# Performance work log

Measured on AMD Instinct MI355X. Metric: run time of the kernel, lower is better.

## Reference

```python
import jax, jax.numpy as jnp
import numpy as np

NUM_HEADS = 16  # init kwarg num_attention_heads


def setup_inputs() -> dict:
    key = jax.random.key(0)
    k1, k2, k3, k4 = jax.random.split(key, 4)
    B, T, E = 2, 2048, 1024
    query = jax.random.normal(k1, (B, T, E), dtype=jnp.float32)
    key_t = jax.random.normal(k2, (B, T, E), dtype=jnp.float32)
    value = jax.random.normal(k3, (B, T, E), dtype=jnp.float32)
    # final output projection (nn.Linear(hidden, hidden, bias=False)); torch stores [out,in]
    W_out = jax.random.normal(k4, (E, E), dtype=jnp.float32) * 0.02
    return {"query": query, "key": key_t, "value": value, "W_out": W_out}


def reference(query, key, value, W_out):
    # NOTE: in the source, the per-head q_i/k_i/v_i linear projections are
    # overwritten by reshapes of the raw inputs, so the qs/ks/vs weights are
    # dead code. Every head computes identical output; mean over heads is a
    # no-op. We reproduce that exact math here.
    B, T, E = query.shape
    H = NUM_HEADS
    d = E // H  # head_dim; also d_k used in the 1/sqrt(d_k) scaling

    def split_heads(x):  # [B,T,E] -> [B,H,T,d]
        return x.reshape(B, T, H, d).transpose(0, 2, 1, 3)

    q = split_heads(query)
    k = split_heads(key)
    v = split_heads(value)

    scale = jnp.sqrt(jnp.asarray(d, dtype=jnp.float32))
    scores = jnp.einsum('bhtd,bhsd->bhts', q, k) / scale  # [B,H,T,T]
    attn = jax.nn.softmax(scores, axis=-1)
    head = jnp.einsum('bhts,bhsd->bhtd', attn, v)         # [B,H,T,d]
    head = head.transpose(0, 2, 1, 3).reshape(B, T, E)    # concat heads

    # mean over H identical head outputs == head; final linear (no bias)
    outputs = head @ W_out.T                              # [B,T,E]
    # mean over H identical attention maps == attn, returned as [B*H,T,T]
    attention = attn.reshape(B * H, T, T)
    return outputs, attention
```

## Files before the change

kernel.cpp:

```cpp
#include <hip/hip_runtime.h>
#include <hip/hip_fp16.h>

#define B_NUM  2
#define T_DIM  2048
#define E_DIM  1024
#define H_NUM  16
#define D_HEAD 64
#define BH_NUM (B_NUM * H_NUM)
#define NT     (T_DIM / 64)

using half8  = __attribute__((ext_vector_type(8))) _Float16;
using half4v = __attribute__((ext_vector_type(4))) _Float16;
using f32x4  = __attribute__((ext_vector_type(4))) float;

#define AS1 __attribute__((address_space(1)))
#define AS3 __attribute__((address_space(3)))

#define QSCALE 0.18033688011112042f

#define BAR_VM(N)                                                       \
    do {                                                                \
        asm volatile("s_waitcnt vmcnt(" #N ")" ::: "memory");           \
        __builtin_amdgcn_s_barrier();                                   \
        __builtin_amdgcn_sched_barrier(0);                              \
    } while (0)

__device__ __forceinline__ void bar_plain() {
    __builtin_amdgcn_s_barrier();
    __builtin_amdgcn_sched_barrier(0);
}

__global__ void cast_all_kernel(const float* __restrict__ kin,
                                const float* __restrict__ win,
                                _Float16* __restrict__ Kh,
                                _Float16* __restrict__ Wh,
                                int nk4, int ntot4) {
    int stride = gridDim.x * blockDim.x;
    for (int i = blockIdx.x * blockDim.x + threadIdx.x; i < ntot4; i += stride) {
        const float* src = (i < nk4) ? kin : win;
        _Float16* dst    = (i < nk4) ? Kh  : Wh;
        int j            = (i < nk4) ? i   : i - nk4;
        float4 v = reinterpret_cast<const float4*>(src)[j];
        half4v h;
        h[0] = (_Float16)v.x; h[1] = (_Float16)v.y;
        h[2] = (_Float16)v.z; h[3] = (_Float16)v.w;
        reinterpret_cast<half4v*>(dst)[j] = h;
    }
}

__global__ void transpose_v_kernel(const float* __restrict__ V,
                                   _Float16* __restrict__ Vt) {
    __shared__ float tile[64][65];
    int s0 = blockIdx.x * 64;
    int bh = blockIdx.y;
    int b = bh >> 4, h = bh & 15;
    int t = threadIdx.x;

    int row = t >> 2;
    int c0  = (t & 3) * 16;
    const float* src = V + ((size_t)(b * T_DIM + s0 + row)) * E_DIM + h * D_HEAD + c0;
#pragma unroll
    for (int j = 0; j < 16; j += 4) {
        float4 v = *reinterpret_cast<const float4*>(src + j);
        tile[row][c0 + j + 0] = v.x;
        tile[row][c0 + j + 1] = v.y;
        tile[row][c0 + j + 2] = v.z;
        tile[row][c0 + j + 3] = v.w;
    }
    __syncthreads();

    int d  = t >> 2;
    int sc = (t & 3) * 16;
    half8 h0, h1;
#pragma unroll
    for (int j = 0; j < 8; ++j) {
        h0[j] = (_Float16)tile[sc + j][d];
        h1[j] = (_Float16)tile[sc + 8 + j][d];
    }
    _Float16* dst = Vt + ((size_t)(bh * D_HEAD + d)) * T_DIM + s0 + sc;
    *reinterpret_cast<half8*>(dst)     = h0;
    *reinterpret_cast<half8*>(dst + 8) = h1;
}

__device__ __forceinline__ void stage_gl(const _Float16* __restrict__ g,
                                         size_t stride, _Float16* lds,
                                         int w, int lane) {
    int r0 = lane >> 3;
    int c  = (lane & 7) ^ r0;
#pragma unroll
    for (int j = 0; j < 2; ++j) {
        int r = (w + 4 * j) * 8 + r0;
        const _Float16* src = g + (size_t)r * stride + c * 8;
        _Float16* dst = lds + (w + 4 * j) * 512;
        __builtin_amdgcn_global_load_lds((const AS1 void*)src, (AS3 void*)dst,
                                         16, 0, 0);
    }
}

__device__ __forceinline__ half8 read_frag64(const _Float16* lds, int row, int chunk) {
    int csw = chunk ^ (row & 7);
    return *reinterpret_cast<const half8*>(lds + row * 64 + csw * 8);
}

__device__ __forceinline__ void load_qfrag(const float* qsrc, int lg, half8* qf) {
#pragma unroll
    for (int ks = 0; ks < 2; ++ks) {
        float4 a0 = *reinterpret_cast<const float4*>(qsrc + (lg + 4 * ks) * 8);
        float4 a1 = *reinterpret_cast<const float4*>(qsrc + (lg + 4 * ks) * 8 + 4);
        qf[ks][0] = (_Float16)(a0.x * QSCALE); qf[ks][1] = (_Float16)(a0.y * QSCALE);
        qf[ks][2] = (_Float16)(a0.z * QSCALE); qf[ks][3] = (_Float16)(a0.w * QSCALE);
        qf[ks][4] = (_Float16)(a1.x * QSCALE); qf[ks][5] = (_Float16)(a1.y * QSCALE);
        qf[ks][6] = (_Float16)(a1.z * QSCALE); qf[ks][7] = (_Float16)(a1.w * QSCALE);
    }
}

__global__ __launch_bounds__(256) void attn_kernel(
        const float* __restrict__ Q, const _Float16* __restrict__ Kh,
        const _Float16* __restrict__ Vt, float* __restrict__ attn_out,
        _Float16* __restrict__ head_h) {
    __shared__ __align__(16) _Float16 kbuf[2][64 * 64];
    __shared__ __align__(16) _Float16 vbuf[2][64 * 64];
    __shared__ __align__(16) _Float16 pbuf[4][16 * 64];

    int tid  = threadIdx.x;
    int wq   = tid >> 6;
    int lane = tid & 63;
    int l15  = lane & 15;
    int lg   = lane >> 4;

    int flat = blockIdx.x;
    int bh   = (flat & 7) * 4 + (flat >> 8);
    int qt   = (flat >> 3) & 31;
    int q0   = qt * 64;
    int b = bh >> 4, h = bh & 15;

    const float* qsrc = Q + ((size_t)(b * T_DIM + q0 + wq * 16 + l15)) * E_DIM + h * D_HEAD;
    half8 qfrag[2];
    load_qfrag(qsrc, lg, qfrag);

    const _Float16* kg = Kh + ((size_t)b * T_DIM) * E_DIM + h * D_HEAD;
    const _Float16* vg = Vt + (size_t)bh * D_HEAD * T_DIM;

#define P1TILE(KB)                                                             \
    {                                                                          \
        f32x4 acc[4];                                                          \
        _Pragma("unroll")                                                      \
        for (int ct = 0; ct < 4; ++ct) acc[ct] = (f32x4){0.f, 0.f, 0.f, 0.f};  \
        _Pragma("unroll")                                                      \
        for (int ks = 0; ks < 2; ++ks)                                         \
            _Pragma("unroll")                                                  \
            for (int ct = 0; ct < 4; ++ct) {                                   \
                half8 kf = read_frag64((KB), ct * 16 + l15, lg + 4 * ks);      \
                acc[ct] = __builtin_amdgcn_mfma_f32_16x16x32_f16(              \
                    kf, qfrag[ks], acc[ct], 0, 0, 0);                          \
            }                                                                  \
        _Pragma("unroll")                                                      \
        for (int ct = 0; ct < 4; ++ct)                                         \
            _Pragma("unroll")                                                  \
            for (int r = 0; r < 4; ++r)                                        \
                lsum += __builtin_amdgcn_exp2f(acc[ct][r]);                    \
    }

    float lsum = 0.0f;
    stage_gl(kg,                        E_DIM, kbuf[0], wq, lane);
    stage_gl(kg + (size_t)64 * E_DIM,   E_DIM, kbuf[1], wq, lane);
    for (int tt = 0; tt < NT / 2; tt += 2) {
        {
            const _Float16* nb = kg + (size_t)(2 * tt + 2) * 64 * E_DIM;
            stage_gl(nb,                      E_DIM, vbuf[0], wq, lane);
            stage_gl(nb + (size_t)64 * E_DIM, E_DIM, vbuf[1], wq, lane);
            BAR_VM(4);
            P1TILE(kbuf[0]);
            P1TILE(kbuf[1]);
            bar_plain();
        }
        {
            if (tt + 2 < NT / 2) {
                const _Float16* nb = kg + (size_t)(2 * tt + 4) * 64 * E_DIM;
                stage_gl(nb,                      E_DIM, kbuf[0], wq, lane);
                stage_gl(nb + (size_t)64 * E_DIM, E_DIM, kbuf[1], wq, lane);
                BAR_VM(4);
            } else {
                BAR_VM(0);
            }
            P1TILE(vbuf[0]);
            P1TILE(vbuf[1]);
            bar_plain();
        }
    }

    lsum += __shfl_xor(lsum, 16);
    lsum += __shfl_xor(lsum, 32);
    float rl = 1.0f / lsum;

    f32x4 oacc[4];
#pragma unroll
    for (int cd = 0; cd < 4; ++cd) oacc[cd] = (f32x4){0.f, 0.f, 0.f, 0.f};

    float* ab = attn_out + (size_t)bh * T_DIM * T_DIM;
    _Float16* pw = pbuf[wq];
    int myq = q0 + wq * 16 + l15;

    int cur = 0;
    stage_gl(kg, E_DIM, kbuf[0], wq, lane);
    stage_gl(vg, T_DIM, vbuf[0], wq, lane);
    for (int t = 0; t < NT; ++t) {
        if (t < NT - 1) {
            stage_gl(kg + (size_t)(t + 1) * 64 * E_DIM, E_DIM, kbuf[cur ^ 1], wq, lane);
            stage_gl(vg + (t + 1) * 64, T_DIM, vbuf[cur ^ 1], wq, lane);
        }
        if (t == 0)           BAR_VM(4);
        else if (t < NT - 1)  BAR_VM(8);
        else                  BAR_VM(4);
        const _Float16* kb = kbuf[cur];
        const _Float16* vb = vbuf[cur];

        f32x4 acc[4];
#pragma unroll
        for (int ct = 0; ct < 4; ++ct) acc[ct] = (f32x4){0.f, 0.f, 0.f, 0.f};
        __builtin_amdgcn_s_setprio(1);
#pragma unroll
        for (int ks = 0; ks < 2; ++ks)
#pragma unroll
            for (int ct = 0; ct < 4; ++ct) {
                half8 kf = read_frag64(kb, ct * 16 + l15, lg + 4 * ks);
                acc[ct] = __builtin_amdgcn_mfma_f32_16x16x32_f16(kf, qfrag[ks], acc[ct], 0, 0, 0);
            }
        __builtin_amdgcn_s_setprio(0);

        float* abrow = ab + (size_t)myq * T_DIM + t * 64 + lg * 4;
#pragma unroll
        for (int ct = 0; ct < 4; ++ct) {
            f32x4 p;
            p[0] = __builtin_amdgcn_exp2f(acc[ct][0]) * rl;
            p[1] = __builtin_amdgcn_exp2f(acc[ct][1]) * rl;
            p[2] = __builtin_amdgcn_exp2f(acc[ct][2]) * rl;
            p[3] = __builtin_amdgcn_exp2f(acc[ct][3]) * rl;
            *reinterpret_cast<f32x4*>(abrow + ct * 16) = p;
            half4v ph;
            ph[0] = (_Float16)p[0]; ph[1] = (_Float16)p[1];
            ph[2] = (_Float16)p[2]; ph[3] = (_Float16)p[3];
            int cc = (ct * 4 + lg) ^ l15;
            *reinterpret_cast<half4v*>(pw + l15 * 64 + cc * 4) = ph;
        }

        __builtin_amdgcn_s_setprio(1);
#pragma unroll
        for (int ks = 0; ks < 2; ++ks) {
            int c0 = 2 * (lg + 4 * ks);
            half4v lo = *reinterpret_cast<const half4v*>(pw + l15 * 64 + ((c0)     ^ l15) * 4);
            half4v hi = *reinterpret_cast<const half4v*>(pw + l15 * 64 + ((c0 + 1) ^ l15) * 4);
            half8 pa;
            pa[0] = lo[0]; pa[1] = lo[1]; pa[2] = lo[2]; pa[3] = lo[3];
            pa[4] = hi[0]; pa[5] = hi[1]; pa[6] = hi[2]; pa[7] = hi[3];
#pragma unroll
            for (int cd = 0; cd < 4; ++cd) {
                half8 vf = read_frag64(vb, cd * 16 + l15, lg + 4 * ks);
                oacc[cd] = __builtin_amdgcn_mfma_f32_16x16x32_f16(pa, vf, oacc[cd], 0, 0, 0);
            }
        }
        __builtin_amdgcn_s_setprio(0);
        bar_plain();
        cur ^= 1;
    }

    _Float16* hw = head_h + ((size_t)(b * T_DIM + q0 + wq * 16)) * E_DIM + h * D_HEAD;
#pragma unroll
    for (int cd = 0; cd < 4; ++cd)
#pragma unroll
        for (int r = 0; r < 4; ++r) {
            int qm = lg * 4 + r;
            hw[(size_t)qm * E_DIM + cd * 16 + l15] = (_Float16)oacc[cd][r];
        }
#undef P1TILE
}

__global__ __launch_bounds__(256) void proj_kernel(
        const _Float16* __restrict__ A, const _Float16* __restrict__ Wh,
        float* __restrict__ out) {
    __shared__ __align__(16) _Float16 abuf[2][64 * 64];
    __shared__ __align__(16) _Float16 bbuf[2][64 * 64];

    int tid  = threadIdx.x;
    int wq   = tid >> 6;
    int lane = tid & 63;
    int l15  = lane & 15;
    int lg   = lane >> 4;

    int m0 = blockIdx.x * 64;
    int n0 = blockIdx.y * 64;

    f32x4 acc[4];
#pragma unroll
    for (int ct = 0; ct < 4; ++ct) acc[ct] = (f32x4){0.f, 0.f, 0.f, 0.f};

    int cur = 0;
    stage_gl(A  + (size_t)m0 * E_DIM, E_DIM, abuf[0], wq, lane);
    stage_gl(Wh + (size_t)n0 * E_DIM, E_DIM, bbuf[0], wq, lane);
    for (int t = 0; t < E_DIM / 64; ++t) {
        if (t + 1 < E_DIM / 64) {
            stage_gl(A  + (size_t)m0 * E_DIM + (t + 1) * 64, E_DIM, abuf[cur ^ 1], wq, lane);
            stage_gl(Wh + (size_t)n0 * E_DIM + (t + 1) * 64, E_DIM, bbuf[cur ^ 1], wq, lane);
            BAR_VM(4);
        } else {
            BAR_VM(0);
        }
#pragma unroll
        for (int ks = 0; ks < 2; ++ks) {
            half8 hf = read_frag64(abuf[cur], wq * 16 + l15, lg + 4 * ks);
#pragma unroll
            for (int ct = 0; ct < 4; ++ct) {
                half8 wf = read_frag64(bbuf[cur], ct * 16 + l15, lg + 4 * ks);
                acc[ct] = __builtin_amdgcn_mfma_f32_16x16x32_f16(wf, hf, acc[ct], 0, 0, 0);
            }
        }
        bar_plain();
        cur ^= 1;
    }

    float* orow = out + (size_t)(m0 + wq * 16 + l15) * E_DIM + n0 + lg * 4;
#pragma unroll
    for (int ct = 0; ct < 4; ++ct) {
        f32x4 o;
        o[0] = acc[ct][0]; o[1] = acc[ct][1]; o[2] = acc[ct][2]; o[3] = acc[ct][3];
        *reinterpret_cast<f32x4*>(orow + ct * 16) = o;
    }
}

extern "C" void kernel_launch(void* const* d_in, const int* in_sizes, int n_in,
                              void* d_out, int out_size, void* d_ws, size_t ws_size,
                              hipStream_t stream) {
    const float* q = (const float*)d_in[0];
    const float* k = (const float*)d_in[1];
    const float* v = (const float*)d_in[2];
    const float* w = (const float*)d_in[3];

    float* outs = (float*)d_out;
    float* attn = outs + (size_t)B_NUM * T_DIM * E_DIM;

    char* ws = (char*)d_ws;
    _Float16* Kh = (_Float16*)(ws);
    _Float16* Vt = (_Float16*)(ws + (size_t)(8  << 20));
    _Float16* Wh = (_Float16*)(ws + (size_t)(16 << 20));
    _Float16* Hh = (_Float16*)(ws + (size_t)(18 << 20));

    int nk4 = B_NUM * T_DIM * E_DIM / 4;
    int nw4 = E_DIM * E_DIM / 4;

    cast_all_kernel<<<1280, 256, 0, stream>>>(k, w, Kh, Wh, nk4, nk4 + nw4);
    transpose_v_kernel<<<dim3(T_DIM / 64, BH_NUM), 256, 0, stream>>>(v, Vt);
    attn_kernel<<<NT * BH_NUM, 256, 0, stream>>>(q, Kh, Vt, attn, Hh);
    proj_kernel<<<dim3((B_NUM * T_DIM) / 64, E_DIM / 64), 256, 0, stream>>>(Hh, Wh, outs);
}
```

Measured before the change: 206.3 us.

## Merge prep kernels, rotate KV tile order per query tile, raise MFMA priority

After: 183.5 us, median of 2. 1.12x faster.

```diff
diff --git a/kernel.cpp b/kernel.cpp
--- a/kernel.cpp
+++ b/kernel.cpp
@@ -30,56 +30,60 @@
     __builtin_amdgcn_sched_barrier(0);
 }
 
-__global__ void cast_all_kernel(const float* __restrict__ kin,
-                                const float* __restrict__ win,
-                                _Float16* __restrict__ Kh,
-                                _Float16* __restrict__ Wh,
-                                int nk4, int ntot4) {
-    int stride = gridDim.x * blockDim.x;
-    for (int i = blockIdx.x * blockDim.x + threadIdx.x; i < ntot4; i += stride) {
-        const float* src = (i < nk4) ? kin : win;
-        _Float16* dst    = (i < nk4) ? Kh  : Wh;
-        int j            = (i < nk4) ? i   : i - nk4;
-        float4 v = reinterpret_cast<const float4*>(src)[j];
-        half4v h;
-        h[0] = (_Float16)v.x; h[1] = (_Float16)v.y;
-        h[2] = (_Float16)v.z; h[3] = (_Float16)v.w;
-        reinterpret_cast<half4v*>(dst)[j] = h;
-    }
-}
-
-__global__ void transpose_v_kernel(const float* __restrict__ V,
-                                   _Float16* __restrict__ Vt) {
+#define TP_BLOCKS  (NT * BH_NUM)
+#define CAST_BLOCKS 1280
+__global__ void prep_kernel(const float* __restrict__ kin,
+                            const float* __restrict__ win,
+                            const float* __restrict__ V,
+                            _Float16* __restrict__ Kh,
+                            _Float16* __restrict__ Wh,
+                            _Float16* __restrict__ Vt,
+                            int nk4, int ntot4) {
     __shared__ float tile[64][65];
-    int s0 = blockIdx.x * 64;
-    int bh = blockIdx.y;
-    int b = bh >> 4, h = bh & 15;
     int t = threadIdx.x;
 
-    int row = t >> 2;
-    int c0  = (t & 3) * 16;
-    const float* src = V + ((size_t)(b * T_DIM + s0 + row)) * E_DIM + h * D_HEAD + c0;
-#pragma unroll
-    for (int j = 0; j < 16; j += 4) {
-        float4 v = *reinterpret_cast<const float4*>(src + j);
-        tile[row][c0 + j + 0] = v.x;
-        tile[row][c0 + j + 1] = v.y;
-        tile[row][c0 + j + 2] = v.z;
-        tile[row][c0 + j + 3] = v.w;
-    }
-    __syncthreads();
-
-    int d  = t >> 2;
-    int sc = (t & 3) * 16;
-    half8 h0, h1;
-#pragma unroll
-    for (int j = 0; j < 8; ++j) {
-        h0[j] = (_Float16)tile[sc + j][d];
-        h1[j] = (_Float16)tile[sc + 8 + j][d];
-    }
-    _Float16* dst = Vt + ((size_t)(bh * D_HEAD + d)) * T_DIM + s0 + sc;
-    *reinterpret_cast<half8*>(dst)     = h0;
-    *reinterpret_cast<half8*>(dst + 8) = h1;
+    if (blockIdx.x < TP_BLOCKS) {
+        int s0 = (blockIdx.x & 31) * 64;
+        int bh = blockIdx.x >> 5;
+        int b = bh >> 4, h = bh & 15;
+
+        int row = t >> 2;
+        int c0  = (t & 3) * 16;
+        const float* src = V + ((size_t)(b * T_DIM + s0 + row)) * E_DIM + h * D_HEAD + c0;
+#pragma unroll
+        for (int j = 0; j < 16; j += 4) {
+            float4 v = *reinterpret_cast<const float4*>(src + j);
+            tile[row][c0 + j + 0] = v.x;
+            tile[row][c0 + j + 1] = v.y;
+            tile[row][c0 + j + 2] = v.z;
+            tile[row][c0 + j + 3] = v.w;
+        }
+        __syncthreads();
+
+        int d  = t >> 2;
+        int sc = (t & 3) * 16;
+        half8 h0, h1;
+#pragma unroll
+        for (int j = 0; j < 8; ++j) {
+            h0[j] = (_Float16)tile[sc + j][d];
+            h1[j] = (_Float16)tile[sc + 8 + j][d];
+        }
+        _Float16* dst = Vt + ((size_t)(bh * D_HEAD + d)) * T_DIM + s0 + sc;
+        *reinterpret_cast<half8*>(dst)     = h0;
+        *reinterpret_cast<half8*>(dst + 8) = h1;
+    } else {
+        int stride = CAST_BLOCKS * 256;
+        for (int i = (blockIdx.x - TP_BLOCKS) * 256 + t; i < ntot4; i += stride) {
+            const float* src = (i < nk4) ? kin : win;
+            _Float16* dst    = (i < nk4) ? Kh  : Wh;
+            int j            = (i < nk4) ? i   : i - nk4;
+            float4 v = reinterpret_cast<const float4*>(src)[j];
+            half4v hh;
+            hh[0] = (_Float16)v.x; hh[1] = (_Float16)v.y;
+            hh[2] = (_Float16)v.z; hh[3] = (_Float16)v.w;
+            reinterpret_cast<half4v*>(dst)[j] = hh;
+        }
+    }
 }
 
 __device__ __forceinline__ void stage_gl(const _Float16* __restrict__ g,
@@ -146,6 +150,7 @@
         f32x4 acc[4];                                                          \
         _Pragma("unroll")                                                      \
         for (int ct = 0; ct < 4; ++ct) acc[ct] = (f32x4){0.f, 0.f, 0.f, 0.f};  \
+        __builtin_amdgcn_s_setprio(1);                                         \
         _Pragma("unroll")                                                      \
         for (int ks = 0; ks < 2; ++ks)                                         \
             _Pragma("unroll")                                                  \
@@ -154,6 +159,7 @@
                 acc[ct] = __builtin_amdgcn_mfma_f32_16x16x32_f16(              \
                     kf, qfrag[ks], acc[ct], 0, 0, 0);                          \
             }                                                                  \
+        __builtin_amdgcn_s_setprio(0);                                         \
         _Pragma("unroll")                                                      \
         for (int ct = 0; ct < 4; ++ct)                                         \
             _Pragma("unroll")                                                  \
@@ -161,14 +167,15 @@
                 lsum += __builtin_amdgcn_exp2f(acc[ct][r]);                    \
     }
 
+    int rot2 = (qt << 1) & 31;
+#define IDX1(n) (((n) + rot2) & 31)
     float lsum = 0.0f;
-    stage_gl(kg,                        E_DIM, kbuf[0], wq, lane);
-    stage_gl(kg + (size_t)64 * E_DIM,   E_DIM, kbuf[1], wq, lane);
+    stage_gl(kg + (size_t)IDX1(0) * 64 * E_DIM, E_DIM, kbuf[0], wq, lane);
+    stage_gl(kg + (size_t)IDX1(1) * 64 * E_DIM, E_DIM, kbuf[1], wq, lane);
     for (int tt = 0; tt < NT / 2; tt += 2) {
         {
-            const _Float16* nb = kg + (size_t)(2 * tt + 2) * 64 * E_DIM;
-            stage_gl(nb,                      E_DIM, vbuf[0], wq, lane);
-            stage_gl(nb + (size_t)64 * E_DIM, E_DIM, vbuf[1], wq, lane);
+            stage_gl(kg + (size_t)IDX1(2 * tt + 2) * 64 * E_DIM, E_DIM, vbuf[0], wq, lane);
+            stage_gl(kg + (size_t)IDX1(2 * tt + 3) * 64 * E_DIM, E_DIM, vbuf[1], wq, lane);
             BAR_VM(4);
             P1TILE(kbuf[0]);
             P1TILE(kbuf[1]);
@@ -176,9 +183,8 @@
         }
         {
             if (tt + 2 < NT / 2) {
-                const _Float16* nb = kg + (size_t)(2 * tt + 4) * 64 * E_DIM;
-                stage_gl(nb,                      E_DIM, kbuf[0], wq, lane);
-                stage_gl(nb + (size_t)64 * E_DIM, E_DIM, kbuf[1], wq, lane);
+                stage_gl(kg + (size_t)IDX1(2 * tt + 4) * 64 * E_DIM, E_DIM, kbuf[0], wq, lane);
+                stage_gl(kg + (size_t)IDX1(2 * tt + 5) * 64 * E_DIM, E_DIM, kbuf[1], wq, lane);
                 BAR_VM(4);
             } else {
                 BAR_VM(0);
@@ -188,6 +194,7 @@
             bar_plain();
         }
     }
+#undef IDX1
 
     lsum += __shfl_xor(lsum, 16);
     lsum += __shfl_xor(lsum, 32);
@@ -202,12 +209,17 @@
     int myq = q0 + wq * 16 + l15;
 
     int cur = 0;
-    stage_gl(kg, E_DIM, kbuf[0], wq, lane);
-    stage_gl(vg, T_DIM, vbuf[0], wq, lane);
+    {
+        int p0 = qt & 31;
+        stage_gl(kg + (size_t)p0 * 64 * E_DIM, E_DIM, kbuf[0], wq, lane);
+        stage_gl(vg + p0 * 64, T_DIM, vbuf[0], wq, lane);
+    }
     for (int t = 0; t < NT; ++t) {
+        int phys = (t + qt) & 31;
         if (t < NT - 1) {
-            stage_gl(kg + (size_t)(t + 1) * 64 * E_DIM, E_DIM, kbuf[cur ^ 1], wq, lane);
-            stage_gl(vg + (t + 1) * 64, T_DIM, vbuf[cur ^ 1], wq, lane);
+            int pn = (t + 1 + qt) & 31;
+            stage_gl(kg + (size_t)pn * 64 * E_DIM, E_DIM, kbuf[cur ^ 1], wq, lane);
+            stage_gl(vg + pn * 64, T_DIM, vbuf[cur ^ 1], wq, lane);
         }
         if (t == 0)           BAR_VM(4);
         else if (t < NT - 1)  BAR_VM(8);
@@ -228,7 +240,7 @@
             }
         __builtin_amdgcn_s_setprio(0);
 
-        float* abrow = ab + (size_t)myq * T_DIM + t * 64 + lg * 4;
+        float* abrow = ab + (size_t)myq * T_DIM + phys * 64 + lg * 4;
 #pragma unroll
         for (int ct = 0; ct < 4; ++ct) {
             f32x4 p;
@@ -347,8 +359,8 @@
     int nk4 = B_NUM * T_DIM * E_DIM / 4;
     int nw4 = E_DIM * E_DIM / 4;
 
-    cast_all_kernel<<<1280, 256, 0, stream>>>(k, w, Kh, Wh, nk4, nk4 + nw4);
-    transpose_v_kernel<<<dim3(T_DIM / 64, BH_NUM), 256, 0, stream>>>(v, Vt);
+    prep_kernel<<<TP_BLOCKS + CAST_BLOCKS, 256, 0, stream>>>(
+        k, w, v, Kh, Wh, Vt, nk4, nk4 + nw4);
     attn_kernel<<<NT * BH_NUM, 256, 0, stream>>>(q, Kh, Vt, attn, Hh);
     proj_kernel<<<dim3((B_NUM * T_DIM) / 64, E_DIM / 64), 256, 0, stream>>>(Hh, Wh, outs);
 }
```
